# Kernel tuning notes

Measured on AMD Instinct MI355X. Metric: run time of the kernel, lower is better.

## Reference

```python
import jax, jax.numpy as jnp
import numpy as np

DIM = 1024
NUM_HEADS = 16
HEAD_DIM = DIM // NUM_HEADS
ROPE_BASE = 10000.0


def _rope_cos_sin(seq_len, head_dim, dtype):
    inv_freq = 1.0 / (ROPE_BASE ** (jnp.arange(0, head_dim, 2, dtype=jnp.float32) / head_dim))
    t = jnp.arange(seq_len, dtype=jnp.float32)
    freqs = jnp.einsum('i,j->ij', t, inv_freq)          # (S, head_dim/2)
    emb = jnp.concatenate([freqs, freqs], axis=-1)       # (S, head_dim)
    return jnp.cos(emb).astype(dtype), jnp.sin(emb).astype(dtype)


def _rotate_half(x):
    x1, x2 = jnp.split(x, 2, axis=-1)
    return jnp.concatenate([-x2, x1], axis=-1)


def setup_inputs() -> dict:
    key = jax.random.key(0)
    k1, k2, k3 = jax.random.split(key, 3)
    B, S = 2, 2048
    x = jax.random.normal(k1, (B, S, DIM), dtype=jnp.float32)
    w_qkv = jax.random.normal(k2, (3 * DIM, DIM), dtype=jnp.float32) * (DIM ** -0.5)
    w_out = jax.random.normal(k3, (DIM, DIM), dtype=jnp.float32) * (DIM ** -0.5)
    return {"x": x, "w_qkv": w_qkv, "w_out": w_out}


def reference(x, w_qkv, w_out):
    B, S, _ = x.shape
    scale = HEAD_DIM ** -0.5

    qkv = jnp.einsum('bsd,ed->bse', x, w_qkv)                 # (B, S, 3*DIM)
    qkv = qkv.reshape(B, S, 3, NUM_HEADS, HEAD_DIM)
    qkv = jnp.transpose(qkv, (2, 0, 3, 1, 4))                  # (3, B, H, S, hd)
    Q, K, V = qkv[0], qkv[1], qkv[2]

    cos, sin = _rope_cos_sin(S, HEAD_DIM, x.dtype)             # (S, hd)
    Q = Q * cos + _rotate_half(Q) * sin
    K = K * cos + _rotate_half(K) * sin

    scores = jnp.einsum('bhqd,bhkd->bhqk', Q, K) * scale       # (B, H, S, S)
    causal = jnp.tril(jnp.ones((S, S), dtype=bool))
    scores = jnp.where(causal[None, None], scores, jnp.asarray(-1e9, scores.dtype))
    attn = jax.nn.softmax(scores, axis=-1)

    out = jnp.einsum('bhqk,bhkd->bhqd', attn, V)               # (B, H, S, hd)
    out = jnp.transpose(out, (0, 2, 1, 3)).reshape(B, S, DIM)
    out = jnp.einsum('bsd,ed->bse', out, w_out)
    return out
```

## Files before the change

kernel.cpp:

```cpp
#include <hip/hip_runtime.h>
#include <hip/hip_bf16.h>

#define DIM 1024
#define NHEADS 16
#define HD 64
#define BB 2
#define SS 2048
#define MTOT (BB*SS)
#define SCALE 0.125f
#define QSCALE 0.1803368801111204f

typedef __attribute__((ext_vector_type(8))) short bf16x8;
typedef __attribute__((ext_vector_type(4))) float f32x4;

__device__ __forceinline__ float bf2f(short u) {
  union { float f; unsigned int i; } v;
  v.i = ((unsigned int)(unsigned short)u) << 16;
  return v.f;
}
__device__ __forceinline__ short f2bf(float f) {
  union { float f; unsigned int i; } v; v.f = f;
  unsigned int r = v.i + 0x7fffu + ((v.i >> 16) & 1u);
  return (short)(r >> 16);
}
__device__ __forceinline__ unsigned int cvtpk_bf16(float lo, float hi) {
  unsigned int r;
  asm("v_cvt_pk_bf16_f32 %0, %1, %2" : "=v"(r) : "v"(lo), "v"(hi));
  return r;
}
__device__ __forceinline__ void async_load16(const short* g, short* l) {
  __builtin_amdgcn_global_load_lds(
      (const __attribute__((address_space(1))) unsigned int*)g,
      (__attribute__((address_space(3))) unsigned int*)l, 16, 0, 0);
}

__global__ void cvt3_kernel(const float* __restrict__ a, short* __restrict__ oa, int na,
                            const float* __restrict__ b, short* __restrict__ ob, int nb,
                            const float* __restrict__ c, short* __restrict__ oc, int nc) {
  int stride = gridDim.x * blockDim.x;
  int tot = na + nb + nc;
  for (int q = blockIdx.x * blockDim.x + threadIdx.x; q < tot; q += stride) {
    const float* src; short* dst; int off;
    if (q < na)            { src = a; dst = oa; off = q; }
    else if (q < na + nb)  { src = b; dst = ob; off = q - na; }
    else                   { src = c; dst = oc; off = q - na - nb; }
    float4 v = *(const float4*)(src + (size_t)off * 4);
    short4 o;
    o.x = f2bf(v.x); o.y = f2bf(v.y); o.z = f2bf(v.z); o.w = f2bf(v.w);
    *(short4*)(dst + (size_t)off * 4) = o;
  }
}

__global__ void rope_table_kernel(float* __restrict__ ct, float* __restrict__ st) {
  int i = blockIdx.x * blockDim.x + threadIdx.x;
  if (i >= SS * 32) return;
  int s = i >> 5, j = i & 31;
  float inv = 1.0f / powf(10000.0f, (float)(2 * j) / 64.0f);
  float ang = (float)s * inv;
  ct[i] = cosf(ang);
  st[i] = sinf(ang);
}

template<bool OUT_F32>
__global__ __launch_bounds__(256) void gemm_bt(
    const short* __restrict__ A, const short* __restrict__ B,
    void* __restrict__ C, int M, int N, int K) {
  __shared__ __align__(16) char smem[16384];
  auto As = reinterpret_cast<short(*)[32]>(smem);
  auto Bs = reinterpret_cast<short(*)[32]>(smem + 8192);
  const int nbx = N >> 7;
  const int chunk = gridDim.x >> 3;
  const int wg = (blockIdx.x & 7) * chunk + (blockIdx.x >> 3);
  const int m0 = (wg / nbx) * 128, n0 = (wg % nbx) * 128;
  const int tid = threadIdx.x;
  const int lane = tid & 63;
  const int wid = tid >> 6;
  const int wm = (wid >> 1) * 64, wn = (wid & 1) * 64;
  const int row = lane & 15, kg = (lane >> 4) * 8;
  const int lrow = lane >> 2;
  const int lcol = (lane & 3) * 8;

  f32x4 acc[4][4];
#pragma unroll
  for (int m = 0; m < 4; m++)
#pragma unroll
    for (int n = 0; n < 4; n++) acc[m][n] = (f32x4){0.f, 0.f, 0.f, 0.f};

  for (int kk = 0; kk < K; kk += 32) {
    __syncthreads();
#pragma unroll
    for (int i = 0; i < 2; i++) {
      int base = i * 64 + wid * 16;
      async_load16(A + (size_t)(m0 + base + lrow) * K + kk + lcol, &As[base][0]);
      async_load16(B + (size_t)(n0 + base + lrow) * K + kk + lcol, &Bs[base][0]);
    }
    __syncthreads();
    bf16x8 af[4], bfr[4];
#pragma unroll
    for (int m = 0; m < 4; m++) af[m] = *(const bf16x8*)(&As[wm + m * 16 + row][kg]);
#pragma unroll
    for (int n = 0; n < 4; n++) bfr[n] = *(const bf16x8*)(&Bs[wn + n * 16 + row][kg]);
#pragma unroll
    for (int m = 0; m < 4; m++)
#pragma unroll
      for (int n = 0; n < 4; n++)
        acc[m][n] = __builtin_amdgcn_mfma_f32_16x16x32_bf16(af[m], bfr[n], acc[m][n], 0, 0, 0);
  }
  float* Lf = (float*)smem;
  const int orow = (lane >> 4) * 4, ocol = lane & 15;
  const int half = wid >> 1;
  const int erow = tid >> 3;
  const int ec = (tid & 7) * 4;
  const int gr_b = m0 + (erow >> 4) * 64 + (erow & 15);
#pragma unroll
  for (int mseg = 0; mseg < 4; mseg++) {
    __syncthreads();
    int rL = half * 16 + orow;
#pragma unroll
    for (int n = 0; n < 4; n++)
#pragma unroll
      for (int r = 0; r < 4; r++)
        Lf[(rL + r) * 128 + wn + n * 16 + ocol] = acc[mseg][n][r];
    __syncthreads();
    int gr = gr_b + mseg * 16;
#pragma unroll
    for (int j = 0; j < 4; j++) {
      float4 v = *(const float4*)&Lf[erow * 128 + ec + j * 32];
      int gc = n0 + ec + j * 32;
      if (OUT_F32) {
        *(float4*)((float*)C + (size_t)gr * N + gc) = v;
      } else {
        union { unsigned int u[2]; short4 s4; } ou;
        ou.u[0] = cvtpk_bf16(v.x, v.y);
        ou.u[1] = cvtpk_bf16(v.z, v.w);
        *(short4*)((short*)C + (size_t)gr * N + gc) = ou.s4;
      }
    }
  }
}

__global__ __launch_bounds__(256) void ropev_kernel(
    const short* __restrict__ qkv, const float* __restrict__ ct, const float* __restrict__ st,
    short* __restrict__ Q, short* __restrict__ K, short* __restrict__ Vt) {
  int bh = blockIdx.y;
  int b = bh >> 4, h = bh & 15;
  int t = threadIdx.x;
  if (blockIdx.x < SS / 64) {
    int s0 = blockIdx.x * 64;
    int rl = t >> 2;
    int d8 = (t & 3) * 8;
    int s = s0 + rl;
    size_t inbase = ((size_t)(b * SS + s)) * 3072 + h * 64 + d8;
    size_t outbase = ((size_t)bh * SS + s) * 64 + d8;
    float c[8], sn[8];
#pragma unroll
    for (int j = 0; j < 8; j++) { c[j] = ct[s * 32 + d8 + j]; sn[j] = st[s * 32 + d8 + j]; }
    {
      bf16x8 x1 = *(const bf16x8*)(qkv + inbase);
      bf16x8 x2 = *(const bf16x8*)(qkv + inbase + 32);
      bf16x8 o1, o2;
#pragma unroll
      for (int j = 0; j < 8; j++) {
        float a = bf2f(x1[j]), bb = bf2f(x2[j]);
        o1[j] = f2bf((a * c[j] - bb * sn[j]) * QSCALE);
        o2[j] = f2bf((bb * c[j] + a * sn[j]) * QSCALE);
      }
      *(bf16x8*)(Q + outbase) = o1;
      *(bf16x8*)(Q + outbase + 32) = o2;
    }
    {
      bf16x8 x1 = *(const bf16x8*)(qkv + inbase + 1024);
      bf16x8 x2 = *(const bf16x8*)(qkv + inbase + 1024 + 32);
      bf16x8 o1, o2;
#pragma unroll
      for (int j = 0; j < 8; j++) {
        float a = bf2f(x1[j]), bb = bf2f(x2[j]);
        o1[j] = f2bf(a * c[j] - bb * sn[j]);
        o2[j] = f2bf(bb * c[j] + a * sn[j]);
      }
      *(bf16x8*)(K + outbase) = o1;
      *(bf16x8*)(K + outbase + 32) = o2;
    }
  } else {
    __shared__ short ls[64][72];
    int s0 = (blockIdx.x - SS / 64) * 64;
#pragma unroll
    for (int p = 0; p < 2; p++) {
      int idx = p * 256 + t;
      int r = idx >> 3, c8 = (idx & 7) * 8;
      *(bf16x8*)(&ls[r][c8]) =
          *(const bf16x8*)(qkv + ((size_t)(b * SS + s0 + r)) * 3072 + 2048 + h * 64 + c8);
    }
    __syncthreads();
    int dl = t >> 2, sg = (t & 3) * 16;
    int c = sg >> 5, hi = (sg >> 4) & 1;
    short tmp[16];
#pragma unroll
    for (int j = 0; j < 16; j++) tmp[j] = ls[sg + j][dl];
    size_t rowbase = ((size_t)bh * 64 + dl) * SS + s0;
#pragma unroll
    for (int g = 0; g < 4; g++) {
      short4 o = { tmp[4 * g], tmp[4 * g + 1], tmp[4 * g + 2], tmp[4 * g + 3] };
      *(short4*)(Vt + rowbase + c * 32 + g * 8 + hi * 4) = o;
    }
  }
}

__global__ __launch_bounds__(256) void attn_kernel(
    const short* __restrict__ Qp, const short* __restrict__ Kp, const short* __restrict__ Vt,
    short* __restrict__ O, float* __restrict__ Pf) {
  __shared__ short Ks[2][64][72];
  __shared__ short Vs[2][64][72];
  int flat = blockIdx.x;
  int wk = (flat & 7) * 128 + (flat >> 3);
  int bh = wk >> 5;
  int sub = wk & 31;
  int pr = sub >> 1, half = sub & 1;
  int b = bh >> 4, h = bh & 15;
  int tid = threadIdx.x, lane = tid & 63, w = tid >> 6;
  int row = lane & 15, grp = lane >> 4;
  const int qtH = 31 - pr;
  const int nseg = 1 + half;

  const int ksr = tid >> 3;
  const int ksc = (tid & 7) * 8;
  const short* Kbase = Kp + (size_t)bh * SS * 64;
  const short* Vbase = Vt + (size_t)bh * 64 * SS;

  bf16x8 kr0, kr1, vr0, vr1;
  auto LOADT = [&](int kv0) {
    kr0 = *(const bf16x8*)(Kbase + (size_t)(kv0 + ksr) * 64 + ksc);
    kr1 = *(const bf16x8*)(Kbase + (size_t)(kv0 + 32 + ksr) * 64 + ksc);
    vr0 = *(const bf16x8*)(Vbase + (size_t)ksr * SS + kv0 + ksc);
    vr1 = *(const bf16x8*)(Vbase + (size_t)(32 + ksr) * SS + kv0 + ksc);
  };
  auto WRITET = [&](int bufi) {
    *(bf16x8*)(&Ks[bufi][ksr][ksc]) = kr0;
    *(bf16x8*)(&Ks[bufi][32 + ksr][ksc]) = kr1;
    *(bf16x8*)(&Vs[bufi][ksr][ksc]) = vr0;
    *(bf16x8*)(&Vs[bufi][32 + ksr][ksc]) = vr1;
  };

  const int kts0 = half ? 16 : 0;
  int cur = 0;
  LOADT(kts0 * 64);
  WRITET(0);
  __syncthreads();

#pragma unroll 1
  for (int s = 0; s < nseg; s++) {
    const int qt  = (s == 0) ? qtH : pr;
    const int kts = (s == 0) ? kts0 : 0;
    const int kte = (s == 0) ? (half ? qtH : 15) : pr;
    const bool fin = (s == 1);
    const int q0 = qt * 64;
    const int q = q0 + w * 16 + row;
    bf16x8 qf0, qf1;
    {
      size_t qb = ((size_t)bh * SS + q) * 64 + grp * 8;
      qf0 = *(const bf16x8*)(Qp + qb);
      qf1 = *(const bf16x8*)(Qp + qb + 32);
    }
    f32x4 acc[4];
#pragma unroll
    for (int d = 0; d < 4; d++) acc[d] = (f32x4){0.f, 0.f, 0.f, 0.f};
    float m = -1e30f, l = 0.f;

#pragma unroll 1
    for (int kt = kts; kt <= kte; kt++) {
      int kv0 = kt * 64;
      bool more = (kt < kte) || (s + 1 < nseg);
      if (more) LOADT(kt < kte ? kv0 + 64 : 0);

      bool last = (kt == qt);
      float sv[4][4];
#pragma unroll
      for (int n = 0; n < 4; n++) {
        if (last && n > w) {
#pragma unroll
          for (int r = 0; r < 4; r++) sv[n][r] = -1e30f;
          continue;
        }
        f32x4 sf = (f32x4){0.f, 0.f, 0.f, 0.f};
        bf16x8 kf0 = *(const bf16x8*)(&Ks[cur][n * 16 + row][grp * 8]);
        bf16x8 kf1 = *(const bf16x8*)(&Ks[cur][n * 16 + row][grp * 8 + 32]);
        sf = __builtin_amdgcn_mfma_f32_16x16x32_bf16(kf0, qf0, sf, 0, 0, 0);
        sf = __builtin_amdgcn_mfma_f32_16x16x32_bf16(kf1, qf1, sf, 0, 0, 0);
#pragma unroll
        for (int r = 0; r < 4; r++) sv[n][r] = sf[r];
      }
      if (last) {
#pragma unroll
        for (int n = 0; n < 4; n++)
#pragma unroll
          for (int r = 0; r < 4; r++) {
            int kv = kv0 + n * 16 + grp * 4 + r;
            if (kv > q) sv[n][r] = -1e30f;
          }
      }
      float pmax = -1e30f;
#pragma unroll
      for (int n = 0; n < 4; n++)
#pragma unroll
        for (int r = 0; r < 4; r++) pmax = fmaxf(pmax, sv[n][r]);
      pmax = fmaxf(pmax, __shfl_xor(pmax, 16));
      pmax = fmaxf(pmax, __shfl_xor(pmax, 32));
      if (__any(pmax - m > 8.f)) {
        float mnew = fmaxf(m, pmax);
        float resc = __builtin_amdgcn_exp2f(m - mnew);
        m = mnew;
        l *= resc;
#pragma unroll
        for (int d = 0; d < 4; d++)
#pragma unroll
          for (int r = 0; r < 4; r++) acc[d][r] *= resc;
      }
      float p[4][4];
      float psum = 0.f;
#pragma unroll
      for (int n = 0; n < 4; n++)
#pragma unroll
        for (int r = 0; r < 4; r++) {
          p[n][r] = __builtin_amdgcn_exp2f(sv[n][r] - m);
          psum += p[n][r];
        }
      psum += __shfl_xor(psum, 16);
      psum += __shfl_xor(psum, 32);
      l += psum;
#pragma unroll
      for (int c = 0; c < 2; c++) {
        union { unsigned int u[4]; bf16x8 v; } pu;
        pu.u[0] = cvtpk_bf16(p[2 * c][0], p[2 * c][1]);
        pu.u[1] = cvtpk_bf16(p[2 * c][2], p[2 * c][3]);
        pu.u[2] = cvtpk_bf16(p[2 * c + 1][0], p[2 * c + 1][1]);
        pu.u[3] = cvtpk_bf16(p[2 * c + 1][2], p[2 * c + 1][3]);
#pragma unroll
        for (int dm = 0; dm < 4; dm++) {
          bf16x8 vf = *(const bf16x8*)(&Vs[cur][dm * 16 + row][c * 32 + grp * 8]);
          acc[dm] = __builtin_amdgcn_mfma_f32_16x16x32_bf16(vf, pu.v, acc[dm], 0, 0, 0);
        }
      }
      if (more) WRITET(cur ^ 1);
      __syncthreads();
      cur ^= 1;
    }
    if (fin) {
      float linv = 1.0f / l;
      size_t ob = ((size_t)(b * SS + q)) * 1024 + h * 64 + grp * 4;
#pragma unroll
      for (int dm = 0; dm < 4; dm++) {
        union { unsigned int u[2]; short4 s4; } ou;
        ou.u[0] = cvtpk_bf16(acc[dm][0] * linv, acc[dm][1] * linv);
        ou.u[1] = cvtpk_bf16(acc[dm][2] * linv, acc[dm][3] * linv);
        *(short4*)(O + ob + dm * 16) = ou.s4;
      }
    } else {
      int slot = (bh * 16 + (qt - 16)) * 2 + half;
      float* P = Pf + (size_t)slot * 64 * 68 + (w * 16 + row) * 68;
#pragma unroll
      for (int dm = 0; dm < 4; dm++) {
        f32x4 a = acc[dm];
        *(float4*)(P + dm * 16 + grp * 4) = *(float4*)&a;
      }
      if (grp == 0) { P[64] = m; P[65] = l; }
    }
  }
}

__global__ __launch_bounds__(64) void merge_kernel(const float* __restrict__ Pf, short* __restrict__ O) {
  int bh = blockIdx.x >> 4, ht = blockIdx.x & 15;
  int b = bh >> 4, h = bh & 15;
  int qt = ht + 16;
  int t = threadIdx.x;
  const float* p0 = Pf + ((size_t)((bh * 16 + ht) * 2)) * 64 * 68 + t * 68;
  const float* p1 = p0 + 64 * 68;
  float m0 = p0[64], l0 = p0[65], m1 = p1[64], l1 = p1[65];
  float mM = fmaxf(m0, m1);
  float e0 = __builtin_amdgcn_exp2f(m0 - mM);
  float e1 = __builtin_amdgcn_exp2f(m1 - mM);
  float linv = 1.0f / (e0 * l0 + e1 * l1);
  size_t ob = ((size_t)(b * SS + qt * 64 + t)) * 1024 + h * 64;
#pragma unroll
  for (int d8 = 0; d8 < 8; d8++) {
    float4 a0 = *(const float4*)(p0 + d8 * 8);
    float4 a1 = *(const float4*)(p1 + d8 * 8);
    float4 b0 = *(const float4*)(p0 + d8 * 8 + 4);
    float4 b1 = *(const float4*)(p1 + d8 * 8 + 4);
    union { unsigned int u[4]; short4 s4[2]; } ou;
    ou.u[0] = cvtpk_bf16((e0 * a0.x + e1 * a1.x) * linv, (e0 * a0.y + e1 * a1.y) * linv);
    ou.u[1] = cvtpk_bf16((e0 * a0.z + e1 * a1.z) * linv, (e0 * a0.w + e1 * a1.w) * linv);
    ou.u[2] = cvtpk_bf16((e0 * b0.x + e1 * b1.x) * linv, (e0 * b0.y + e1 * b1.y) * linv);
    ou.u[3] = cvtpk_bf16((e0 * b0.z + e1 * b1.z) * linv, (e0 * b0.w + e1 * b1.w) * linv);
    *(short4*)(O + ob + d8 * 8) = ou.s4[0];
    *(short4*)(O + ob + d8 * 8 + 4) = ou.s4[1];
  }
}

extern "C" void kernel_launch(void* const* d_in, const int* in_sizes, int n_in,
                              void* d_out, int out_size, void* d_ws, size_t ws_size,
                              hipStream_t stream) {
  (void)in_sizes; (void)n_in; (void)out_size; (void)ws_size;
  const float* x     = (const float*)d_in[0];
  const float* w_qkv = (const float*)d_in[1];
  const float* w_out = (const float*)d_in[2];
  float* out = (float*)d_out;

  char* ws = (char*)d_ws;
  size_t off = 0;
  auto alloc = [&](size_t bytes) -> void* {
    void* p = ws + off;
    off += (bytes + 255) & ~(size_t)255;
    return p;
  };
  short* xb    = (short*)alloc((size_t)MTOT * DIM * 2);
  short* wqkvb = (short*)alloc((size_t)3072 * 1024 * 2);
  short* woutb = (short*)alloc((size_t)1024 * 1024 * 2);
  short* qkvb  = (short*)alloc((size_t)MTOT * 3072 * 2);
  short* Qb    = (short*)alloc((size_t)32 * SS * 64 * 2);
  short* Kb    = (short*)alloc((size_t)32 * SS * 64 * 2);
  short* Vtb   = (short*)alloc((size_t)32 * 64 * SS * 2);
  float* ct    = (float*)alloc((size_t)SS * 32 * 4);
  float* st    = (float*)alloc((size_t)SS * 32 * 4);
  short* attnb = xb;
  float* Pf    = (float*)qkvb;

  cvt3_kernel<<<2048, 256, 0, stream>>>(x, xb, MTOT * DIM / 4,
                                        w_qkv, wqkvb, 3072 * 1024 / 4,
                                        w_out, woutb, 1024 * 1024 / 4);
  rope_table_kernel<<<SS * 32 / 256, 256, 0, stream>>>(ct, st);
  gemm_bt<false><<<(3072 / 128) * (MTOT / 128), 256, 0, stream>>>(xb, wqkvb, qkvb, MTOT, 3072, 1024);
  ropev_kernel<<<dim3(2 * SS / 64, 32), 256, 0, stream>>>(qkvb, ct, st, Qb, Kb, Vtb);
  attn_kernel<<<1024, 256, 0, stream>>>(Qb, Kb, Vtb, attnb, Pf);
  merge_kernel<<<512, 64, 0, stream>>>(Pf, attnb);
  gemm_bt<true><<<(1024 / 128) * (MTOT / 128), 256, 0, stream>>>(attnb, woutb, out, MTOT, 1024, 1024);
}
```

Before: 139.1 us.

## Fold rope table into convert kernel, simplify GEMM epilogue, single-buffer attention

The rope cos/sin table is now computed inside the fp32-to-bf16 conversion kernel, which removes one launch. The GEMM epilogue drops its LDS-staged coalesced store and writes scalar elements straight from the accumulators. The attention kernel goes from double-buffered to single-buffered K/V LDS, gains a launch bound of 8 blocks per SM and uses s_setprio around the MFMA sections. The scalar uncoalesced GEMM stores and the loss of overlap between LDS writes and compute could hurt, while the smaller LDS footprint allows higher occupancy.

```diff
diff --git a/kernel.cpp b/kernel.cpp
--- a/kernel.cpp
+++ b/kernel.cpp
@@ -36,10 +36,19 @@
 
 __global__ void cvt3_kernel(const float* __restrict__ a, short* __restrict__ oa, int na,
                             const float* __restrict__ b, short* __restrict__ ob, int nb,
-                            const float* __restrict__ c, short* __restrict__ oc, int nc) {
+                            const float* __restrict__ c, short* __restrict__ oc, int nc,
+                            float* __restrict__ ct, float* __restrict__ st) {
+  int gid = blockIdx.x * blockDim.x + threadIdx.x;
+  if (gid < SS * 32) {
+    int s = gid >> 5, j = gid & 31;
+    float inv = 1.0f / powf(10000.0f, (float)(2 * j) / 64.0f);
+    float ang = (float)s * inv;
+    ct[gid] = cosf(ang);
+    st[gid] = sinf(ang);
+  }
   int stride = gridDim.x * blockDim.x;
   int tot = na + nb + nc;
-  for (int q = blockIdx.x * blockDim.x + threadIdx.x; q < tot; q += stride) {
+  for (int q = gid; q < tot; q += stride) {
     const float* src; short* dst; int off;
     if (q < na)            { src = a; dst = oa; off = q; }
     else if (q < na + nb)  { src = b; dst = ob; off = q - na; }
@@ -51,23 +60,12 @@
   }
 }
 
-__global__ void rope_table_kernel(float* __restrict__ ct, float* __restrict__ st) {
-  int i = blockIdx.x * blockDim.x + threadIdx.x;
-  if (i >= SS * 32) return;
-  int s = i >> 5, j = i & 31;
-  float inv = 1.0f / powf(10000.0f, (float)(2 * j) / 64.0f);
-  float ang = (float)s * inv;
-  ct[i] = cosf(ang);
-  st[i] = sinf(ang);
-}
-
 template<bool OUT_F32>
 __global__ __launch_bounds__(256) void gemm_bt(
     const short* __restrict__ A, const short* __restrict__ B,
     void* __restrict__ C, int M, int N, int K) {
-  __shared__ __align__(16) char smem[16384];
-  auto As = reinterpret_cast<short(*)[32]>(smem);
-  auto Bs = reinterpret_cast<short(*)[32]>(smem + 8192);
+  __shared__ __align__(16) short As[128][32];
+  __shared__ __align__(16) short Bs[128][32];
   const int nbx = N >> 7;
   const int chunk = gridDim.x >> 3;
   const int wg = (blockIdx.x & 7) * chunk + (blockIdx.x >> 3);
@@ -106,37 +104,18 @@
       for (int n = 0; n < 4; n++)
         acc[m][n] = __builtin_amdgcn_mfma_f32_16x16x32_bf16(af[m], bfr[n], acc[m][n], 0, 0, 0);
   }
-  float* Lf = (float*)smem;
   const int orow = (lane >> 4) * 4, ocol = lane & 15;
-  const int half = wid >> 1;
-  const int erow = tid >> 3;
-  const int ec = (tid & 7) * 4;
-  const int gr_b = m0 + (erow >> 4) * 64 + (erow & 15);
-#pragma unroll
-  for (int mseg = 0; mseg < 4; mseg++) {
-    __syncthreads();
-    int rL = half * 16 + orow;
+#pragma unroll
+  for (int m = 0; m < 4; m++)
 #pragma unroll
     for (int n = 0; n < 4; n++)
 #pragma unroll
-      for (int r = 0; r < 4; r++)
-        Lf[(rL + r) * 128 + wn + n * 16 + ocol] = acc[mseg][n][r];
-    __syncthreads();
-    int gr = gr_b + mseg * 16;
-#pragma unroll
-    for (int j = 0; j < 4; j++) {
-      float4 v = *(const float4*)&Lf[erow * 128 + ec + j * 32];
-      int gc = n0 + ec + j * 32;
-      if (OUT_F32) {
-        *(float4*)((float*)C + (size_t)gr * N + gc) = v;
-      } else {
-        union { unsigned int u[2]; short4 s4; } ou;
-        ou.u[0] = cvtpk_bf16(v.x, v.y);
-        ou.u[1] = cvtpk_bf16(v.z, v.w);
-        *(short4*)((short*)C + (size_t)gr * N + gc) = ou.s4;
-      }
-    }
-  }
+      for (int r = 0; r < 4; r++) {
+        int gr = m0 + wm + m * 16 + orow + r;
+        int gc = n0 + wn + n * 16 + ocol;
+        if (OUT_F32) ((float*)C)[(size_t)gr * N + gc] = acc[m][n][r];
+        else         ((short*)C)[(size_t)gr * N + gc] = f2bf(acc[m][n][r]);
+      }
 }
 
 __global__ __launch_bounds__(256) void ropev_kernel(
@@ -206,11 +185,11 @@
   }
 }
 
-__global__ __launch_bounds__(256) void attn_kernel(
+__global__ __launch_bounds__(256, 8) void attn_kernel(
     const short* __restrict__ Qp, const short* __restrict__ Kp, const short* __restrict__ Vt,
     short* __restrict__ O, float* __restrict__ Pf) {
-  __shared__ short Ks[2][64][72];
-  __shared__ short Vs[2][64][72];
+  __shared__ short Ks[64][72];
+  __shared__ short Vs[64][72];
   int flat = blockIdx.x;
   int wk = (flat & 7) * 128 + (flat >> 3);
   int bh = wk >> 5;
@@ -234,18 +213,15 @@
     vr0 = *(const bf16x8*)(Vbase + (size_t)ksr * SS + kv0 + ksc);
     vr1 = *(const bf16x8*)(Vbase + (size_t)(32 + ksr) * SS + kv0 + ksc);
   };
-  auto WRITET = [&](int bufi) {
-    *(bf16x8*)(&Ks[bufi][ksr][ksc]) = kr0;
-    *(bf16x8*)(&Ks[bufi][32 + ksr][ksc]) = kr1;
-    *(bf16x8*)(&Vs[bufi][ksr][ksc]) = vr0;
-    *(bf16x8*)(&Vs[bufi][32 + ksr][ksc]) = vr1;
+  auto WRITET = [&]() {
+    *(bf16x8*)(&Ks[ksr][ksc]) = kr0;
+    *(bf16x8*)(&Ks[32 + ksr][ksc]) = kr1;
+    *(bf16x8*)(&Vs[ksr][ksc]) = vr0;
+    *(bf16x8*)(&Vs[32 + ksr][ksc]) = vr1;
   };
 
   const int kts0 = half ? 16 : 0;
-  int cur = 0;
   LOADT(kts0 * 64);
-  WRITET(0);
-  __syncthreads();
 
 #pragma unroll 1
   for (int s = 0; s < nseg; s++) {
@@ -270,10 +246,13 @@
     for (int kt = kts; kt <= kte; kt++) {
       int kv0 = kt * 64;
       bool more = (kt < kte) || (s + 1 < nseg);
+      WRITET();
+      __syncthreads();
       if (more) LOADT(kt < kte ? kv0 + 64 : 0);
 
       bool last = (kt == qt);
       float sv[4][4];
+      __builtin_amdgcn_s_setprio(1);
 #pragma unroll
       for (int n = 0; n < 4; n++) {
         if (last && n > w) {
@@ -282,13 +261,14 @@
           continue;
         }
         f32x4 sf = (f32x4){0.f, 0.f, 0.f, 0.f};
-        bf16x8 kf0 = *(const bf16x8*)(&Ks[cur][n * 16 + row][grp * 8]);
-        bf16x8 kf1 = *(const bf16x8*)(&Ks[cur][n * 16 + row][grp * 8 + 32]);
+        bf16x8 kf0 = *(const bf16x8*)(&Ks[n * 16 + row][grp * 8]);
+        bf16x8 kf1 = *(const bf16x8*)(&Ks[n * 16 + row][grp * 8 + 32]);
         sf = __builtin_amdgcn_mfma_f32_16x16x32_bf16(kf0, qf0, sf, 0, 0, 0);
         sf = __builtin_amdgcn_mfma_f32_16x16x32_bf16(kf1, qf1, sf, 0, 0, 0);
 #pragma unroll
         for (int r = 0; r < 4; r++) sv[n][r] = sf[r];
       }
+      __builtin_amdgcn_s_setprio(0);
       if (last) {
 #pragma unroll
         for (int n = 0; n < 4; n++)
@@ -327,6 +307,7 @@
       psum += __shfl_xor(psum, 16);
       psum += __shfl_xor(psum, 32);
       l += psum;
+      __builtin_amdgcn_s_setprio(1);
 #pragma unroll
       for (int c = 0; c < 2; c++) {
         union { unsigned int u[4]; bf16x8 v; } pu;
@@ -336,13 +317,12 @@
         pu.u[3] = cvtpk_bf16(p[2 * c + 1][2], p[2 * c + 1][3]);
 #pragma unroll
         for (int dm = 0; dm < 4; dm++) {
-          bf16x8 vf = *(const bf16x8*)(&Vs[cur][dm * 16 + row][c * 32 + grp * 8]);
+          bf16x8 vf = *(const bf16x8*)(&Vs[dm * 16 + row][c * 32 + grp * 8]);
           acc[dm] = __builtin_amdgcn_mfma_f32_16x16x32_bf16(vf, pu.v, acc[dm], 0, 0, 0);
         }
       }
-      if (more) WRITET(cur ^ 1);
+      __builtin_amdgcn_s_setprio(0);
       __syncthreads();
-      cur ^= 1;
     }
     if (fin) {
       float linv = 1.0f / l;
@@ -426,8 +406,7 @@
 
   cvt3_kernel<<<2048, 256, 0, stream>>>(x, xb, MTOT * DIM / 4,
                                         w_qkv, wqkvb, 3072 * 1024 / 4,
-                                        w_out, woutb, 1024 * 1024 / 4);
-  rope_table_kernel<<<SS * 32 / 256, 256, 0, stream>>>(ct, st);
+                                        w_out, woutb, 1024 * 1024 / 4, ct, st);
   gemm_bt<false><<<(3072 / 128) * (MTOT / 128), 256, 0, stream>>>(xb, wqkvb, qkvb, MTOT, 3072, 1024);
   ropev_kernel<<<dim3(2 * SS / 64, 32), 256, 0, stream>>>(qkvb, ct, st, Qb, Kb, Vtb);
   attn_kernel<<<1024, 256, 0, stream>>>(Qb, Kb, Vtb, attnb, Pf);
```

Measured after the change: 171.6 us. 1.23x slower.
